# Kernel optimization log

Hardware: AMD Instinct MI355X
Metric: run time of the kernel (lower is better)

## Reference

```python
import jax, jax.numpy as jnp
import numpy as np

N_NODES = 100000
N_EDGES = 3200000
IN_CH, HID, OUT_CH = 512, 16, 64


def gcn_conv(x, src, dst, W, b, n_nodes):
    """GCNConv: x @ W, then sym-normalized aggregation with self-loops."""
    xw = x @ W  # [N, F_out]
    loop = jnp.arange(n_nodes, dtype=src.dtype)
    s = jnp.concatenate([src, loop])  # sources (messages gathered here)
    d = jnp.concatenate([dst, loop])  # targets (messages scattered here)
    deg = jax.ops.segment_sum(jnp.ones_like(d, dtype=xw.dtype), d, num_segments=n_nodes)
    dinv = jnp.where(deg > 0, jax.lax.rsqrt(deg), 0.0)
    norm = dinv[s] * dinv[d]  # [E+N]
    msgs = xw[s] * norm[:, None]  # gather + scale
    out = jax.ops.segment_sum(msgs, d, num_segments=n_nodes)
    return out + b


def setup_inputs() -> dict:
    key = jax.random.key(0)
    k1, k2, k3, k4, k5 = jax.random.split(key, 5)
    x = jax.random.normal(k1, (N_NODES, IN_CH), dtype=jnp.float32)
    edge_index = jax.random.randint(k2, (2, N_EDGES), 0, N_NODES, dtype=jnp.int32)
    # Glorot-style init for GCNConv linear weights, zero bias (PyG default)
    W1 = jax.random.normal(k3, (IN_CH, HID), dtype=jnp.float32) * (1.0 / np.sqrt(IN_CH))
    b1 = jnp.zeros((HID,), dtype=jnp.float32)
    W2 = jax.random.normal(k4, (HID, OUT_CH), dtype=jnp.float32) * (1.0 / np.sqrt(HID))
    b2 = jnp.zeros((OUT_CH,), dtype=jnp.float32)
    return {"x": x, "edge_index": edge_index, "W1": W1, "b1": b1, "W2": W2, "b2": b2}


def reference(x, edge_index, W1, b1, W2, b2):
    # eval mode: dropout(p=0.5) is identity
    src, dst = edge_index[0], edge_index[1]
    h = gcn_conv(x, src, dst, W1, b1, N_NODES)
    h = jax.nn.relu(h)
    out = gcn_conv(h, src, dst, W2, b2, N_NODES)
    return out
```

## Files before the change

### kernel.cpp

```cpp
#include <hip/hip_runtime.h>

#define N_NODES 100000
#define N_EDGES 3200000
#define IN_CH 512
#define HID 16
#define OUT_CH 64

#define NB1 98
#define CAP1 34816
#define LEAF 64
#define CAP2 2560
#define NLEAF 1563
#define NLEAF_SLOTS (NB1 * 16)
#define BIN1_CHUNK 4096
#define BIN1_BLOCKS ((N_EDGES + BIN1_CHUNK - 1) / BIN1_CHUNK)
#define BIN2_SPLIT 9
#define BIN2_CHUNK 3872

__device__ __forceinline__ float4 f4add(float4 a, float4 b) {
    return float4{a.x + b.x, a.y + b.y, a.z + b.z, a.w + b.w};
}
__device__ __forceinline__ float4 f4fma(float s, float4 w, float4 a) {
    return float4{a.x + s * w.x, a.y + s * w.y, a.z + s * w.z, a.w + s * w.w};
}


__global__ void k_init_bcur(int* bcur1, int* bcur2) {
    int i = blockIdx.x * blockDim.x + threadIdx.x;
    if (i < NB1) bcur1[i] = i * CAP1;
    if (i < NLEAF_SLOTS) bcur2[i] = i * CAP2;
}


__global__ __launch_bounds__(256) void k_bin1(const int* __restrict__ src,
                                              const int* __restrict__ dst,
                                              int* __restrict__ pairs1,
                                              int* __restrict__ bcur1) {
    __shared__ int cnt[NB1];
    __shared__ int base[NB1];
    const int tid = threadIdx.x;
    const int lo = blockIdx.x * BIN1_CHUNK;
    const int hi = min(lo + BIN1_CHUNK, N_EDGES);
    if (tid < NB1) cnt[tid] = 0;
    __syncthreads();
    for (int i = lo + tid; i < hi; i += 256) {
        int d = __builtin_nontemporal_load(dst + i);
        atomicAdd(&cnt[d >> 10], 1);
    }
    __syncthreads();
    if (tid < NB1 && cnt[tid] > 0) base[tid] = atomicAdd(&bcur1[tid], cnt[tid]);
    __syncthreads();
    if (tid < NB1) cnt[tid] = 0;
    __syncthreads();
    for (int i = lo + tid; i < hi; i += 256) {
        int d = __builtin_nontemporal_load(dst + i);
        int s = __builtin_nontemporal_load(src + i);
        int b = d >> 10;
        int r = atomicAdd(&cnt[b], 1);
        pairs1[base[b] + r] = (s << 10) | (d & 1023);
    }
}


__global__ __launch_bounds__(256) void k_bin2(const int* __restrict__ pairs1,
                                              const int* __restrict__ bcur1,
                                              int* __restrict__ pairs2,
                                              int* __restrict__ bcur2) {
    __shared__ int cnt[16];
    __shared__ int base[16];
    const int b = blockIdx.x / BIN2_SPLIT;
    const int s = blockIdx.x % BIN2_SPLIT;
    const int tid = threadIdx.x;
    const int len = bcur1[b] - b * CAP1;
    const int lo = b * CAP1 + min(s * BIN2_CHUNK, len);
    const int hi = b * CAP1 + min((s + 1) * BIN2_CHUNK, len);
    if (tid < 16) cnt[tid] = 0;
    __syncthreads();
    for (int i = lo + tid; i < hi; i += 256)
        atomicAdd(&cnt[(pairs1[i] & 1023) >> 6], 1);
    __syncthreads();
    if (tid < 16 && cnt[tid] > 0) base[tid] = atomicAdd(&bcur2[b * 16 + tid], cnt[tid]);
    __syncthreads();
    if (tid < 16) cnt[tid] = 0;
    __syncthreads();
    for (int i = lo + tid; i < hi; i += 256) {
        int e = pairs1[i];
        int l = (e & 1023) >> 6;
        int r = atomicAdd(&cnt[l], 1);
        pairs2[base[l] + r] = e;
    }
}


__global__ __launch_bounds__(256) void k_leafscan(const int* __restrict__ bcur2,
                                                  int* __restrict__ leafoff) {
    __shared__ int sm[256];
    __shared__ int carry;
    const int tid = threadIdx.x;
    if (tid == 0) carry = 0;
    __syncthreads();
    for (int r = 0; r < (NLEAF_SLOTS + 255) / 256; ++r) {
        int idx = r * 256 + tid;
        int v = (idx < NLEAF_SLOTS) ? (bcur2[idx] - idx * CAP2) : 0;
        sm[tid] = v;
        __syncthreads();
        for (int st = 1; st < 256; st <<= 1) {
            int t = (tid >= st) ? sm[tid - st] : 0;
            __syncthreads();
            sm[tid] += t;
            __syncthreads();
        }
        if (idx < NLEAF_SLOTS) leafoff[idx] = carry + sm[tid] - v;
        int tot = sm[255];
        __syncthreads();
        if (tid == 0) carry += tot;
        __syncthreads();
    }
}


__global__ __launch_bounds__(256) void k_scatter2(const int* __restrict__ pairs2,
                                                  const int* __restrict__ bcur2,
                                                  const int* __restrict__ leafoff,
                                                  int* __restrict__ off,
                                                  int* __restrict__ deg,
                                                  float* __restrict__ dinv,
                                                  int* __restrict__ csr) {
    __shared__ int cnt[LEAF];
    __shared__ int lcur[LEAF];
    __shared__ int buf[CAP2];
    const int leaf = blockIdx.x;
    const int tid = threadIdx.x;
    const int base2 = leaf * CAP2;
    const int len = min(bcur2[leaf] - base2, CAP2);
    const int obase = leafoff[leaf];
    if (tid < LEAF) cnt[tid] = 0;
    __syncthreads();
    for (int i = tid; i < len; i += 256)
        atomicAdd(&cnt[pairs2[base2 + i] & 63], 1);
    __syncthreads();
    if (tid < LEAF) {
        int v = cnt[tid];
        int s = v;
        for (int d = 1; d < LEAF; d <<= 1) {
            int t = __shfl_up(s, d, 64);
            if (tid >= d) s += t;
        }
        int excl = s - v;
        lcur[tid] = excl;
        int node = leaf * LEAF + tid;
        if (node < N_NODES) {
            off[node] = obase + excl;
            deg[node] = 1 + v;
            dinv[node] = rsqrtf((float)(1 + v));
        }
    }
    __syncthreads();
    for (int i = tid; i < len; i += 256) {
        int e = pairs2[base2 + i];
        int p = atomicAdd(&lcur[e & 63], 1);
        buf[p] = e >> 10;
    }
    __syncthreads();
    for (int i = tid; i < len; i += 256)
        csr[obase + i] = buf[i];
}


#define G1_BS 256
#define G1_NODES 128
#define G1_KT 64
#define G1_STRIDE (G1_KT + 4)

__global__ __launch_bounds__(G1_BS) void k_gemm1(const float* __restrict__ x,
                                                 const float* __restrict__ W1,
                                                 const float* __restrict__ dinv,
                                                 float* __restrict__ y1) {
    __shared__ float xt[G1_NODES * G1_STRIDE];
    __shared__ float wt[G1_KT * HID];
    const int tid = threadIdx.x;
    const int nl = tid >> 2;
    const int cg = tid & 3;
    const int node_base = blockIdx.x * G1_NODES;

    float4 acc0 = {0.f, 0.f, 0.f, 0.f};
    float4 acc1 = {0.f, 0.f, 0.f, 0.f};

    for (int kt = 0; kt < IN_CH; kt += G1_KT) {
        __syncthreads();
        for (int j = 0; j < 8; ++j) {
            int f4 = j * G1_BS + tid;
            int r = f4 >> 4;
            int c4 = f4 & 15;
            int gr = node_base + r;
            float4 v = {0.f, 0.f, 0.f, 0.f};
            if (gr < N_NODES)
                v = *(const float4*)(x + (size_t)gr * IN_CH + kt + c4 * 4);
            *(float4*)(xt + r * G1_STRIDE + c4 * 4) = v;
        }
        {
            int r = tid >> 2;
            int c4 = tid & 3;
            *(float4*)(wt + r * HID + c4 * 4) =
                *(const float4*)(W1 + (size_t)(kt + r) * HID + c4 * 4);
        }
        __syncthreads();

        for (int kk = 0; kk < G1_KT; kk += 4) {
            float4 x0 = *(const float4*)(xt + nl * G1_STRIDE + kk);
            float4 x1 = *(const float4*)(xt + (nl + 64) * G1_STRIDE + kk);
            float4 w0 = *(const float4*)(wt + (kk + 0) * HID + cg * 4);
            float4 w1 = *(const float4*)(wt + (kk + 1) * HID + cg * 4);
            float4 w2 = *(const float4*)(wt + (kk + 2) * HID + cg * 4);
            float4 w3 = *(const float4*)(wt + (kk + 3) * HID + cg * 4);
            acc0 = f4fma(x0.x, w0, acc0); acc0 = f4fma(x0.y, w1, acc0);
            acc0 = f4fma(x0.z, w2, acc0); acc0 = f4fma(x0.w, w3, acc0);
            acc1 = f4fma(x1.x, w0, acc1); acc1 = f4fma(x1.y, w1, acc1);
            acc1 = f4fma(x1.z, w2, acc1); acc1 = f4fma(x1.w, w3, acc1);
        }
    }

    int n0 = node_base + nl;
    int n1 = n0 + 64;
    if (n0 < N_NODES) {
        float dv = dinv[n0];
        float4 o = {acc0.x * dv, acc0.y * dv, acc0.z * dv, acc0.w * dv};
        *(float4*)(y1 + (size_t)n0 * HID + cg * 4) = o;
    }
    if (n1 < N_NODES) {
        float dv = dinv[n1];
        float4 o = {acc1.x * dv, acc1.y * dv, acc1.z * dv, acc1.w * dv};
        *(float4*)(y1 + (size_t)n1 * HID + cg * 4) = o;
    }
}


__global__ __launch_bounds__(256) void k_layer1(const float* __restrict__ y1,
                                                const int* __restrict__ off,
                                                const int* __restrict__ deg,
                                                const int* __restrict__ csr,
                                                const float* __restrict__ dinv,
                                                const float* __restrict__ b1,
                                                float* __restrict__ y2) {
    int t = blockIdx.x * blockDim.x + threadIdx.x;
    int n = t >> 2;
    int cg = t & 3;
    if (n >= N_NODES) return;
    int base = off[n];
    int cnt = deg[n] - 1;
    float4 a0 = {0,0,0,0}, a1 = {0,0,0,0}, a2 = {0,0,0,0}, a3 = {0,0,0,0};
    int p = 0;
    for (; p + 4 <= cnt; p += 4) {
        int s0 = csr[base + p + 0];
        int s1 = csr[base + p + 1];
        int s2 = csr[base + p + 2];
        int s3 = csr[base + p + 3];
        a0 = f4add(a0, *(const float4*)(y1 + (size_t)s0 * HID + cg * 4));
        a1 = f4add(a1, *(const float4*)(y1 + (size_t)s1 * HID + cg * 4));
        a2 = f4add(a2, *(const float4*)(y1 + (size_t)s2 * HID + cg * 4));
        a3 = f4add(a3, *(const float4*)(y1 + (size_t)s3 * HID + cg * 4));
    }
    for (; p < cnt; ++p)
        a0 = f4add(a0, *(const float4*)(y1 + (size_t)csr[base + p] * HID + cg * 4));
    float4 acc = f4add(f4add(a0, a1), f4add(a2, a3));
    float dv = dinv[n];
    float4 self = *(const float4*)(y1 + (size_t)n * HID + cg * 4);
    float4 b = ((const float4*)b1)[cg];
    float4 h;
    h.x = fmaxf(dv * (acc.x + self.x) + b.x, 0.f) * dv;
    h.y = fmaxf(dv * (acc.y + self.y) + b.y, 0.f) * dv;
    h.z = fmaxf(dv * (acc.z + self.z) + b.z, 0.f) * dv;
    h.w = fmaxf(dv * (acc.w + self.w) + b.w, 0.f) * dv;
    *(float4*)(y2 + (size_t)n * HID + cg * 4) = h;
}


__global__ __launch_bounds__(256) void k_layer2(const float* __restrict__ y2,
                                                const int* __restrict__ off,
                                                const int* __restrict__ deg,
                                                const int* __restrict__ csr,
                                                const float* __restrict__ dinv,
                                                const float* __restrict__ W2,
                                                const float* __restrict__ b2,
                                                float* __restrict__ out) {
    __shared__ float w2[HID * OUT_CH];
    __shared__ float bs[OUT_CH];
    int tid = threadIdx.x;
    for (int j = tid; j < HID * OUT_CH; j += 256) w2[j] = W2[j];
    if (tid < OUT_CH) bs[tid] = b2[tid];
    __syncthreads();

    int t = blockIdx.x * blockDim.x + tid;
    int n = t >> 2;
    int cg = t & 3;
    if (n >= N_NODES) return;
    int base = off[n];
    int cnt = deg[n] - 1;
    float4 a0 = {0,0,0,0}, a1 = {0,0,0,0}, a2 = {0,0,0,0}, a3 = {0,0,0,0};
    int p = 0;
    for (; p + 4 <= cnt; p += 4) {
        int s0 = csr[base + p + 0];
        int s1 = csr[base + p + 1];
        int s2 = csr[base + p + 2];
        int s3 = csr[base + p + 3];
        a0 = f4add(a0, *(const float4*)(y2 + (size_t)s0 * HID + cg * 4));
        a1 = f4add(a1, *(const float4*)(y2 + (size_t)s1 * HID + cg * 4));
        a2 = f4add(a2, *(const float4*)(y2 + (size_t)s2 * HID + cg * 4));
        a3 = f4add(a3, *(const float4*)(y2 + (size_t)s3 * HID + cg * 4));
    }
    for (; p < cnt; ++p)
        a0 = f4add(a0, *(const float4*)(y2 + (size_t)csr[base + p] * HID + cg * 4));
    float4 acc = f4add(f4add(a0, a1), f4add(a2, a3));
    float dv = dinv[n];
    float4 self = *(const float4*)(y2 + (size_t)n * HID + cg * 4);
    float4 z4 = {dv * (acc.x + self.x), dv * (acc.y + self.y),
                 dv * (acc.z + self.z), dv * (acc.w + self.w)};

    int lane = tid & 63;
    int lbase = lane & ~3;
    float z[16];
    for (int j = 0; j < 4; ++j) {
        z[j * 4 + 0] = __shfl(z4.x, lbase + j, 64);
        z[j * 4 + 1] = __shfl(z4.y, lbase + j, 64);
        z[j * 4 + 2] = __shfl(z4.z, lbase + j, 64);
        z[j * 4 + 3] = __shfl(z4.w, lbase + j, 64);
    }

    float4 o0 = ((const float4*)bs)[cg * 4 + 0];
    float4 o1 = ((const float4*)bs)[cg * 4 + 1];
    float4 o2 = ((const float4*)bs)[cg * 4 + 2];
    float4 o3 = ((const float4*)bs)[cg * 4 + 3];
    for (int cc = 0; cc < HID; ++cc) {
        const float* wr = w2 + cc * OUT_CH + cg * 16;
        float zz = z[cc];
        o0 = f4fma(zz, *(const float4*)(wr + 0), o0);
        o1 = f4fma(zz, *(const float4*)(wr + 4), o1);
        o2 = f4fma(zz, *(const float4*)(wr + 8), o2);
        o3 = f4fma(zz, *(const float4*)(wr + 12), o3);
    }
    float* orow = out + (size_t)n * OUT_CH + cg * 16;
    *(float4*)(orow + 0) = o0;
    *(float4*)(orow + 4) = o1;
    *(float4*)(orow + 8) = o2;
    *(float4*)(orow + 12) = o3;
}


extern "C" void kernel_launch(void* const* d_in, const int* in_sizes, int n_in,
                              void* d_out, int out_size, void* d_ws, size_t ws_size,
                              hipStream_t stream) {
    const float* x  = (const float*)d_in[0];
    const int*   ei = (const int*)d_in[1];
    const float* W1 = (const float*)d_in[2];
    const float* b1 = (const float*)d_in[3];
    const float* W2 = (const float*)d_in[4];
    const float* b2 = (const float*)d_in[5];
    float* out = (float*)d_out;

    const int* src = ei;
    const int* dst = ei + N_EDGES;

    char* w = (char*)d_ws;
    const size_t SN = 409600;
    int*   deg      = (int*)(w);
    float* dinv     = (float*)(w + SN);
    int*   off      = (int*)(w + 2 * SN);
    int*   bcur1    = (int*)(w + 3 * SN);
    int*   bcur2    = (int*)(w + 3 * SN + 8192);
    int*   leafoff  = (int*)(w + 3 * SN + 16384);
    char*  regB     = w + 4 * SN;
    int*   pairs1   = (int*)regB;
    int*   csr      = (int*)regB;
    char*  regC     = regB + (size_t)NB1 * CAP1 * 4;
    int*   pairs2   = (int*)regC;
    float* y1       = (float*)regC;
    float* y2       = (float*)(regC + 6553600);

    k_init_bcur<<<(NLEAF_SLOTS + 255) / 256, 256, 0, stream>>>(bcur1, bcur2);
    k_bin1<<<BIN1_BLOCKS, 256, 0, stream>>>(src, dst, pairs1, bcur1);
    k_bin2<<<NB1 * BIN2_SPLIT, 256, 0, stream>>>(pairs1, bcur1, pairs2, bcur2);
    k_leafscan<<<1, 256, 0, stream>>>(bcur2, leafoff);
    k_scatter2<<<NLEAF, 256, 0, stream>>>(pairs2, bcur2, leafoff, off, deg, dinv, csr);
    k_gemm1<<<(N_NODES + G1_NODES - 1) / G1_NODES, G1_BS, 0, stream>>>(x, W1, dinv, y1);
    k_layer1<<<(N_NODES * 4 + 255) / 256, 256, 0, stream>>>(y1, off, deg, csr, dinv, b1, y2);
    k_layer2<<<(N_NODES * 4 + 255) / 256, 256, 0, stream>>>(y2, off, deg, csr, dinv, W2, b2, out);
}
```

Measured before the change: 248.5 us.

## Split hidden features into two half-width arrays for cache-resident gather aggregation

Stores the 16-wide layer-1 projection as two separate 8-float arrays (3.2 MB each), so each aggregation pass gathers from a smaller table that can stay resident in cache. Each layer's aggregation is run as two passes, one per half, and the layer-2 W2 projection moves into a separate GEMM kernel that reads an intermediate z buffer. The deg array is dropped in favour of off[n+1]-off[n] plus an inline rsqrt. The cost is re-reading the CSR index array twice per layer, extra kernel launches, and an extra write and read of z.

```diff
diff --git a/kernel.cpp b/kernel.cpp
--- a/kernel.cpp
+++ b/kernel.cpp
@@ -25,10 +25,11 @@
 }
 
 
-__global__ void k_init_bcur(int* bcur1, int* bcur2) {
+__global__ void k_init_bcur(int* bcur1, int* bcur2, int* off) {
     int i = blockIdx.x * blockDim.x + threadIdx.x;
     if (i < NB1) bcur1[i] = i * CAP1;
     if (i < NLEAF_SLOTS) bcur2[i] = i * CAP2;
+    if (i == 0) off[N_NODES] = N_EDGES;
 }
 
 
@@ -123,7 +124,6 @@
                                                   const int* __restrict__ bcur2,
                                                   const int* __restrict__ leafoff,
                                                   int* __restrict__ off,
-                                                  int* __restrict__ deg,
                                                   float* __restrict__ dinv,
                                                   int* __restrict__ csr) {
     __shared__ int cnt[LEAF];
@@ -151,7 +151,6 @@
         int node = leaf * LEAF + tid;
         if (node < N_NODES) {
             off[node] = obase + excl;
-            deg[node] = 1 + v;
             dinv[node] = rsqrtf((float)(1 + v));
         }
     }
@@ -175,13 +174,16 @@
 __global__ __launch_bounds__(G1_BS) void k_gemm1(const float* __restrict__ x,
                                                  const float* __restrict__ W1,
                                                  const float* __restrict__ dinv,
-                                                 float* __restrict__ y1) {
+                                                 float* __restrict__ y1a,
+                                                 float* __restrict__ y1b) {
     __shared__ float xt[G1_NODES * G1_STRIDE];
     __shared__ float wt[G1_KT * HID];
     const int tid = threadIdx.x;
     const int nl = tid >> 2;
     const int cg = tid & 3;
     const int node_base = blockIdx.x * G1_NODES;
+    float* yh = (cg & 2) ? y1b : y1a;
+    const int hc = (cg & 1) * 4;
 
     float4 acc0 = {0.f, 0.f, 0.f, 0.f};
     float4 acc1 = {0.f, 0.f, 0.f, 0.f};
@@ -225,29 +227,28 @@
     if (n0 < N_NODES) {
         float dv = dinv[n0];
         float4 o = {acc0.x * dv, acc0.y * dv, acc0.z * dv, acc0.w * dv};
-        *(float4*)(y1 + (size_t)n0 * HID + cg * 4) = o;
+        *(float4*)(yh + (size_t)n0 * 8 + hc) = o;
     }
     if (n1 < N_NODES) {
         float dv = dinv[n1];
         float4 o = {acc1.x * dv, acc1.y * dv, acc1.z * dv, acc1.w * dv};
-        *(float4*)(y1 + (size_t)n1 * HID + cg * 4) = o;
-    }
-}
-
-
-__global__ __launch_bounds__(256) void k_layer1(const float* __restrict__ y1,
-                                                const int* __restrict__ off,
-                                                const int* __restrict__ deg,
-                                                const int* __restrict__ csr,
-                                                const float* __restrict__ dinv,
-                                                const float* __restrict__ b1,
-                                                float* __restrict__ y2) {
+        *(float4*)(yh + (size_t)n1 * 8 + hc) = o;
+    }
+}
+
+
+__global__ __launch_bounds__(256) void k_agg1(const float* __restrict__ yh,
+                                              const int* __restrict__ off,
+                                              const int* __restrict__ csr,
+                                              const float* __restrict__ b1,
+                                              const int half,
+                                              float* __restrict__ y2h) {
     int t = blockIdx.x * blockDim.x + threadIdx.x;
-    int n = t >> 2;
-    int cg = t & 3;
+    int n = t >> 1;
     if (n >= N_NODES) return;
+    int hc = (t & 1) * 4;
     int base = off[n];
-    int cnt = deg[n] - 1;
+    int cnt = off[n + 1] - base;
     float4 a0 = {0,0,0,0}, a1 = {0,0,0,0}, a2 = {0,0,0,0}, a3 = {0,0,0,0};
     int p = 0;
     for (; p + 4 <= cnt; p += 4) {
@@ -255,47 +256,37 @@
         int s1 = csr[base + p + 1];
         int s2 = csr[base + p + 2];
         int s3 = csr[base + p + 3];
-        a0 = f4add(a0, *(const float4*)(y1 + (size_t)s0 * HID + cg * 4));
-        a1 = f4add(a1, *(const float4*)(y1 + (size_t)s1 * HID + cg * 4));
-        a2 = f4add(a2, *(const float4*)(y1 + (size_t)s2 * HID + cg * 4));
-        a3 = f4add(a3, *(const float4*)(y1 + (size_t)s3 * HID + cg * 4));
+        a0 = f4add(a0, *(const float4*)(yh + (size_t)s0 * 8 + hc));
+        a1 = f4add(a1, *(const float4*)(yh + (size_t)s1 * 8 + hc));
+        a2 = f4add(a2, *(const float4*)(yh + (size_t)s2 * 8 + hc));
+        a3 = f4add(a3, *(const float4*)(yh + (size_t)s3 * 8 + hc));
     }
     for (; p < cnt; ++p)
-        a0 = f4add(a0, *(const float4*)(y1 + (size_t)csr[base + p] * HID + cg * 4));
+        a0 = f4add(a0, *(const float4*)(yh + (size_t)csr[base + p] * 8 + hc));
     float4 acc = f4add(f4add(a0, a1), f4add(a2, a3));
-    float dv = dinv[n];
-    float4 self = *(const float4*)(y1 + (size_t)n * HID + cg * 4);
-    float4 b = ((const float4*)b1)[cg];
+    float dv = rsqrtf((float)(cnt + 1));
+    float4 self = *(const float4*)(yh + (size_t)n * 8 + hc);
+    float4 b = *(const float4*)(b1 + half * 8 + hc);
     float4 h;
     h.x = fmaxf(dv * (acc.x + self.x) + b.x, 0.f) * dv;
     h.y = fmaxf(dv * (acc.y + self.y) + b.y, 0.f) * dv;
     h.z = fmaxf(dv * (acc.z + self.z) + b.z, 0.f) * dv;
     h.w = fmaxf(dv * (acc.w + self.w) + b.w, 0.f) * dv;
-    *(float4*)(y2 + (size_t)n * HID + cg * 4) = h;
-}
-
-
-__global__ __launch_bounds__(256) void k_layer2(const float* __restrict__ y2,
-                                                const int* __restrict__ off,
-                                                const int* __restrict__ deg,
-                                                const int* __restrict__ csr,
-                                                const float* __restrict__ dinv,
-                                                const float* __restrict__ W2,
-                                                const float* __restrict__ b2,
-                                                float* __restrict__ out) {
-    __shared__ float w2[HID * OUT_CH];
-    __shared__ float bs[OUT_CH];
-    int tid = threadIdx.x;
-    for (int j = tid; j < HID * OUT_CH; j += 256) w2[j] = W2[j];
-    if (tid < OUT_CH) bs[tid] = b2[tid];
-    __syncthreads();
-
-    int t = blockIdx.x * blockDim.x + tid;
-    int n = t >> 2;
-    int cg = t & 3;
+    *(float4*)(y2h + (size_t)n * 8 + hc) = h;
+}
+
+
+__global__ __launch_bounds__(256) void k_agg2(const float* __restrict__ yh,
+                                              const int* __restrict__ off,
+                                              const int* __restrict__ csr,
+                                              const int half,
+                                              float* __restrict__ z) {
+    int t = blockIdx.x * blockDim.x + threadIdx.x;
+    int n = t >> 1;
     if (n >= N_NODES) return;
+    int hc = (t & 1) * 4;
     int base = off[n];
-    int cnt = deg[n] - 1;
+    int cnt = off[n + 1] - base;
     float4 a0 = {0,0,0,0}, a1 = {0,0,0,0}, a2 = {0,0,0,0}, a3 = {0,0,0,0};
     int p = 0;
     for (; p + 4 <= cnt; p += 4) {
@@ -303,42 +294,57 @@
         int s1 = csr[base + p + 1];
         int s2 = csr[base + p + 2];
         int s3 = csr[base + p + 3];
-        a0 = f4add(a0, *(const float4*)(y2 + (size_t)s0 * HID + cg * 4));
-        a1 = f4add(a1, *(const float4*)(y2 + (size_t)s1 * HID + cg * 4));
-        a2 = f4add(a2, *(const float4*)(y2 + (size_t)s2 * HID + cg * 4));
-        a3 = f4add(a3, *(const float4*)(y2 + (size_t)s3 * HID + cg * 4));
+        a0 = f4add(a0, *(const float4*)(yh + (size_t)s0 * 8 + hc));
+        a1 = f4add(a1, *(const float4*)(yh + (size_t)s1 * 8 + hc));
+        a2 = f4add(a2, *(const float4*)(yh + (size_t)s2 * 8 + hc));
+        a3 = f4add(a3, *(const float4*)(yh + (size_t)s3 * 8 + hc));
     }
     for (; p < cnt; ++p)
-        a0 = f4add(a0, *(const float4*)(y2 + (size_t)csr[base + p] * HID + cg * 4));
+        a0 = f4add(a0, *(const float4*)(yh + (size_t)csr[base + p] * 8 + hc));
     float4 acc = f4add(f4add(a0, a1), f4add(a2, a3));
-    float dv = dinv[n];
-    float4 self = *(const float4*)(y2 + (size_t)n * HID + cg * 4);
-    float4 z4 = {dv * (acc.x + self.x), dv * (acc.y + self.y),
+    float dv = rsqrtf((float)(cnt + 1));
+    float4 self = *(const float4*)(yh + (size_t)n * 8 + hc);
+    float4 zv = {dv * (acc.x + self.x), dv * (acc.y + self.y),
                  dv * (acc.z + self.z), dv * (acc.w + self.w)};
-
-    int lane = tid & 63;
-    int lbase = lane & ~3;
-    float z[16];
-    for (int j = 0; j < 4; ++j) {
-        z[j * 4 + 0] = __shfl(z4.x, lbase + j, 64);
-        z[j * 4 + 1] = __shfl(z4.y, lbase + j, 64);
-        z[j * 4 + 2] = __shfl(z4.z, lbase + j, 64);
-        z[j * 4 + 3] = __shfl(z4.w, lbase + j, 64);
-    }
-
-    float4 o0 = ((const float4*)bs)[cg * 4 + 0];
-    float4 o1 = ((const float4*)bs)[cg * 4 + 1];
-    float4 o2 = ((const float4*)bs)[cg * 4 + 2];
-    float4 o3 = ((const float4*)bs)[cg * 4 + 3];
+    *(float4*)(z + (size_t)n * HID + half * 8 + hc) = zv;
+}
+
+
+__global__ __launch_bounds__(256) void k_gemm2(const float* __restrict__ z,
+                                               const float* __restrict__ W2,
+                                               const float* __restrict__ b2,
+                                               float* __restrict__ out) {
+    __shared__ float w2[HID * OUT_CH];
+    __shared__ float bs[OUT_CH];
+    int tid = threadIdx.x;
+    for (int j = tid; j < HID * OUT_CH; j += 256) w2[j] = W2[j];
+    if (tid < OUT_CH) bs[tid] = b2[tid];
+    __syncthreads();
+
+    int t = blockIdx.x * blockDim.x + tid;
+    int n = t >> 2;
+    int q = t & 3;
+    if (n >= N_NODES) return;
+    const float* zr = z + (size_t)n * HID;
+    float4 z0 = *(const float4*)(zr + 0);
+    float4 z1 = *(const float4*)(zr + 4);
+    float4 z2 = *(const float4*)(zr + 8);
+    float4 z3 = *(const float4*)(zr + 12);
+    float zz[16] = {z0.x, z0.y, z0.z, z0.w, z1.x, z1.y, z1.z, z1.w,
+                    z2.x, z2.y, z2.z, z2.w, z3.x, z3.y, z3.z, z3.w};
+    float4 o0 = ((const float4*)bs)[q * 4 + 0];
+    float4 o1 = ((const float4*)bs)[q * 4 + 1];
+    float4 o2 = ((const float4*)bs)[q * 4 + 2];
+    float4 o3 = ((const float4*)bs)[q * 4 + 3];
     for (int cc = 0; cc < HID; ++cc) {
-        const float* wr = w2 + cc * OUT_CH + cg * 16;
-        float zz = z[cc];
-        o0 = f4fma(zz, *(const float4*)(wr + 0), o0);
-        o1 = f4fma(zz, *(const float4*)(wr + 4), o1);
-        o2 = f4fma(zz, *(const float4*)(wr + 8), o2);
-        o3 = f4fma(zz, *(const float4*)(wr + 12), o3);
-    }
-    float* orow = out + (size_t)n * OUT_CH + cg * 16;
+        const float* wr = w2 + cc * OUT_CH + q * 16;
+        float s = zz[cc];
+        o0 = f4fma(s, *(const float4*)(wr + 0), o0);
+        o1 = f4fma(s, *(const float4*)(wr + 4), o1);
+        o2 = f4fma(s, *(const float4*)(wr + 8), o2);
+        o3 = f4fma(s, *(const float4*)(wr + 12), o3);
+    }
+    float* orow = out + (size_t)n * OUT_CH + q * 16;
     *(float4*)(orow + 0) = o0;
     *(float4*)(orow + 4) = o1;
     *(float4*)(orow + 8) = o2;
@@ -362,26 +368,34 @@
 
     char* w = (char*)d_ws;
     const size_t SN = 409600;
-    int*   deg      = (int*)(w);
-    float* dinv     = (float*)(w + SN);
-    int*   off      = (int*)(w + 2 * SN);
-    int*   bcur1    = (int*)(w + 3 * SN);
-    int*   bcur2    = (int*)(w + 3 * SN + 8192);
-    int*   leafoff  = (int*)(w + 3 * SN + 16384);
-    char*  regB     = w + 4 * SN;
+    float* dinv     = (float*)(w);
+    int*   off      = (int*)(w + SN);
+    int*   bcur1    = (int*)(w + 2 * SN);
+    int*   bcur2    = (int*)(w + 2 * SN + 8192);
+    int*   leafoff  = (int*)(w + 2 * SN + 16384);
+    char*  regB     = w + 3 * SN;
     int*   pairs1   = (int*)regB;
     int*   csr      = (int*)regB;
     char*  regC     = regB + (size_t)NB1 * CAP1 * 4;
     int*   pairs2   = (int*)regC;
-    float* y1       = (float*)regC;
-    float* y2       = (float*)(regC + 6553600);
-
-    k_init_bcur<<<(NLEAF_SLOTS + 255) / 256, 256, 0, stream>>>(bcur1, bcur2);
+    float* y1a      = (float*)regC;
+    float* y1b      = (float*)(regC + 3200000);
+    float* z        = (float*)(regC + 6400000);
+    char*  regD     = regC + (size_t)NLEAF_SLOTS * CAP2 * 4;
+    float* y2a      = (float*)regD;
+    float* y2b      = (float*)(regD + 3200000);
+
+    const int aggGrid = (N_NODES * 2 + 255) / 256;
+
+    k_init_bcur<<<(NLEAF_SLOTS + 255) / 256, 256, 0, stream>>>(bcur1, bcur2, off);
     k_bin1<<<BIN1_BLOCKS, 256, 0, stream>>>(src, dst, pairs1, bcur1);
     k_bin2<<<NB1 * BIN2_SPLIT, 256, 0, stream>>>(pairs1, bcur1, pairs2, bcur2);
     k_leafscan<<<1, 256, 0, stream>>>(bcur2, leafoff);
-    k_scatter2<<<NLEAF, 256, 0, stream>>>(pairs2, bcur2, leafoff, off, deg, dinv, csr);
-    k_gemm1<<<(N_NODES + G1_NODES - 1) / G1_NODES, G1_BS, 0, stream>>>(x, W1, dinv, y1);
-    k_layer1<<<(N_NODES * 4 + 255) / 256, 256, 0, stream>>>(y1, off, deg, csr, dinv, b1, y2);
-    k_layer2<<<(N_NODES * 4 + 255) / 256, 256, 0, stream>>>(y2, off, deg, csr, dinv, W2, b2, out);
-}
+    k_scatter2<<<NLEAF, 256, 0, stream>>>(pairs2, bcur2, leafoff, off, dinv, csr);
+    k_gemm1<<<(N_NODES + G1_NODES - 1) / G1_NODES, G1_BS, 0, stream>>>(x, W1, dinv, y1a, y1b);
+    k_agg1<<<aggGrid, 256, 0, stream>>>(y1a, off, csr, b1, 0, y2a);
+    k_agg1<<<aggGrid, 256, 0, stream>>>(y1b, off, csr, b1, 1, y2b);
+    k_agg2<<<aggGrid, 256, 0, stream>>>(y2a, off, csr, 0, z);
+    k_agg2<<<aggGrid, 256, 0, stream>>>(y2b, off, csr, 1, z);
+    k_gemm2<<<(N_NODES * 4 + 255) / 256, 256, 0, stream>>>(z, W2, b2, out);
+}
```

After: 287.8 us. +15.8%, slower.

## Store hidden features as bf16 and derive degree from CSR offsets

Applied to the files above, without the earlier changes.

Intermediate node features y1 and y2 are packed to bf16 with round-to-nearest-even, which halves the bytes moved by the random gathers in both aggregation layers. The separate degree and dinv arrays are dropped from the layer kernels: the count comes from off[n+1]-off[n] and rsqrt is recomputed in place, with a sentinel written at off[N_NODES]. Nontemporal stores are used for the outputs. Accuracy drops to bf16 precision for the intermediate features.

```diff
diff --git a/kernel.cpp b/kernel.cpp
--- a/kernel.cpp
+++ b/kernel.cpp
@@ -17,18 +17,34 @@
 #define BIN2_SPLIT 9
 #define BIN2_CHUNK 3872
 
-__device__ __forceinline__ float4 f4add(float4 a, float4 b) {
-    return float4{a.x + b.x, a.y + b.y, a.z + b.z, a.w + b.w};
-}
-__device__ __forceinline__ float4 f4fma(float s, float4 w, float4 a) {
-    return float4{a.x + s * w.x, a.y + s * w.y, a.z + s * w.z, a.w + s * w.w};
-}
-
-
-__global__ void k_init_bcur(int* bcur1, int* bcur2) {
+typedef float f4 __attribute__((ext_vector_type(4)));
+typedef unsigned int v2u __attribute__((ext_vector_type(2)));
+
+__device__ __forceinline__ unsigned rne(float f) {
+    unsigned u = __float_as_uint(f);
+    return (u + 0x7fffu + ((u >> 16) & 1u)) >> 16;
+}
+__device__ __forceinline__ v2u pk4(f4 f) {
+    v2u r;
+    r.x = rne(f.x) | (rne(f.y) << 16);
+    r.y = rne(f.z) | (rne(f.w) << 16);
+    return r;
+}
+__device__ __forceinline__ f4 up4(v2u v) {
+    f4 r;
+    r.x = __uint_as_float(v.x << 16);
+    r.y = __uint_as_float(v.x & 0xffff0000u);
+    r.z = __uint_as_float(v.y << 16);
+    r.w = __uint_as_float(v.y & 0xffff0000u);
+    return r;
+}
+
+
+__global__ void k_init_bcur(int* bcur1, int* bcur2, int* off) {
     int i = blockIdx.x * blockDim.x + threadIdx.x;
     if (i < NB1) bcur1[i] = i * CAP1;
     if (i < NLEAF_SLOTS) bcur2[i] = i * CAP2;
+    if (i == 0) off[N_NODES] = N_EDGES;
 }
 
 
@@ -123,7 +139,6 @@
                                                   const int* __restrict__ bcur2,
                                                   const int* __restrict__ leafoff,
                                                   int* __restrict__ off,
-                                                  int* __restrict__ deg,
                                                   float* __restrict__ dinv,
                                                   int* __restrict__ csr) {
     __shared__ int cnt[LEAF];
@@ -151,7 +166,6 @@
         int node = leaf * LEAF + tid;
         if (node < N_NODES) {
             off[node] = obase + excl;
-            deg[node] = 1 + v;
             dinv[node] = rsqrtf((float)(1 + v));
         }
     }
@@ -175,7 +189,7 @@
 __global__ __launch_bounds__(G1_BS) void k_gemm1(const float* __restrict__ x,
                                                  const float* __restrict__ W1,
                                                  const float* __restrict__ dinv,
-                                                 float* __restrict__ y1) {
+                                                 unsigned short* __restrict__ y1) {
     __shared__ float xt[G1_NODES * G1_STRIDE];
     __shared__ float wt[G1_KT * HID];
     const int tid = threadIdx.x;
@@ -183,40 +197,40 @@
     const int cg = tid & 3;
     const int node_base = blockIdx.x * G1_NODES;
 
-    float4 acc0 = {0.f, 0.f, 0.f, 0.f};
-    float4 acc1 = {0.f, 0.f, 0.f, 0.f};
+    f4 acc0 = {0.f, 0.f, 0.f, 0.f};
+    f4 acc1 = {0.f, 0.f, 0.f, 0.f};
 
     for (int kt = 0; kt < IN_CH; kt += G1_KT) {
         __syncthreads();
         for (int j = 0; j < 8; ++j) {
-            int f4 = j * G1_BS + tid;
-            int r = f4 >> 4;
-            int c4 = f4 & 15;
+            int f = j * G1_BS + tid;
+            int r = f >> 4;
+            int c4 = f & 15;
             int gr = node_base + r;
-            float4 v = {0.f, 0.f, 0.f, 0.f};
+            f4 v = {0.f, 0.f, 0.f, 0.f};
             if (gr < N_NODES)
-                v = *(const float4*)(x + (size_t)gr * IN_CH + kt + c4 * 4);
-            *(float4*)(xt + r * G1_STRIDE + c4 * 4) = v;
+                v = *(const f4*)(x + (size_t)gr * IN_CH + kt + c4 * 4);
+            *(f4*)(xt + r * G1_STRIDE + c4 * 4) = v;
         }
         {
             int r = tid >> 2;
             int c4 = tid & 3;
-            *(float4*)(wt + r * HID + c4 * 4) =
-                *(const float4*)(W1 + (size_t)(kt + r) * HID + c4 * 4);
+            *(f4*)(wt + r * HID + c4 * 4) =
+                *(const f4*)(W1 + (size_t)(kt + r) * HID + c4 * 4);
         }
         __syncthreads();
 
         for (int kk = 0; kk < G1_KT; kk += 4) {
-            float4 x0 = *(const float4*)(xt + nl * G1_STRIDE + kk);
-            float4 x1 = *(const float4*)(xt + (nl + 64) * G1_STRIDE + kk);
-            float4 w0 = *(const float4*)(wt + (kk + 0) * HID + cg * 4);
-            float4 w1 = *(const float4*)(wt + (kk + 1) * HID + cg * 4);
-            float4 w2 = *(const float4*)(wt + (kk + 2) * HID + cg * 4);
-            float4 w3 = *(const float4*)(wt + (kk + 3) * HID + cg * 4);
-            acc0 = f4fma(x0.x, w0, acc0); acc0 = f4fma(x0.y, w1, acc0);
-            acc0 = f4fma(x0.z, w2, acc0); acc0 = f4fma(x0.w, w3, acc0);
-            acc1 = f4fma(x1.x, w0, acc1); acc1 = f4fma(x1.y, w1, acc1);
-            acc1 = f4fma(x1.z, w2, acc1); acc1 = f4fma(x1.w, w3, acc1);
+            f4 x0 = *(const f4*)(xt + nl * G1_STRIDE + kk);
+            f4 x1 = *(const f4*)(xt + (nl + 64) * G1_STRIDE + kk);
+            f4 w0 = *(const f4*)(wt + (kk + 0) * HID + cg * 4);
+            f4 w1 = *(const f4*)(wt + (kk + 1) * HID + cg * 4);
+            f4 w2 = *(const f4*)(wt + (kk + 2) * HID + cg * 4);
+            f4 w3 = *(const f4*)(wt + (kk + 3) * HID + cg * 4);
+            acc0 += x0.x * w0; acc0 += x0.y * w1;
+            acc0 += x0.z * w2; acc0 += x0.w * w3;
+            acc1 += x1.x * w0; acc1 += x1.y * w1;
+            acc1 += x1.z * w2; acc1 += x1.w * w3;
         }
     }
 
@@ -224,62 +238,58 @@
     int n1 = n0 + 64;
     if (n0 < N_NODES) {
         float dv = dinv[n0];
-        float4 o = {acc0.x * dv, acc0.y * dv, acc0.z * dv, acc0.w * dv};
-        *(float4*)(y1 + (size_t)n0 * HID + cg * 4) = o;
+        __builtin_nontemporal_store(pk4(acc0 * dv),
+            (v2u*)(y1 + (size_t)n0 * HID + cg * 4));
     }
     if (n1 < N_NODES) {
         float dv = dinv[n1];
-        float4 o = {acc1.x * dv, acc1.y * dv, acc1.z * dv, acc1.w * dv};
-        *(float4*)(y1 + (size_t)n1 * HID + cg * 4) = o;
-    }
-}
-
-
-__global__ __launch_bounds__(256) void k_layer1(const float* __restrict__ y1,
+        __builtin_nontemporal_store(pk4(acc1 * dv),
+            (v2u*)(y1 + (size_t)n1 * HID + cg * 4));
+    }
+}
+
+
+__global__ __launch_bounds__(256) void k_layer1(const unsigned short* __restrict__ y1,
                                                 const int* __restrict__ off,
-                                                const int* __restrict__ deg,
                                                 const int* __restrict__ csr,
-                                                const float* __restrict__ dinv,
                                                 const float* __restrict__ b1,
-                                                float* __restrict__ y2) {
+                                                unsigned short* __restrict__ y2) {
     int t = blockIdx.x * blockDim.x + threadIdx.x;
     int n = t >> 2;
     int cg = t & 3;
     if (n >= N_NODES) return;
     int base = off[n];
-    int cnt = deg[n] - 1;
-    float4 a0 = {0,0,0,0}, a1 = {0,0,0,0}, a2 = {0,0,0,0}, a3 = {0,0,0,0};
+    int cnt = off[n + 1] - base;
+    f4 a0 = {0,0,0,0}, a1 = {0,0,0,0}, a2 = {0,0,0,0}, a3 = {0,0,0,0};
     int p = 0;
     for (; p + 4 <= cnt; p += 4) {
         int s0 = csr[base + p + 0];
         int s1 = csr[base + p + 1];
         int s2 = csr[base + p + 2];
         int s3 = csr[base + p + 3];
-        a0 = f4add(a0, *(const float4*)(y1 + (size_t)s0 * HID + cg * 4));
-        a1 = f4add(a1, *(const float4*)(y1 + (size_t)s1 * HID + cg * 4));
-        a2 = f4add(a2, *(const float4*)(y1 + (size_t)s2 * HID + cg * 4));
-        a3 = f4add(a3, *(const float4*)(y1 + (size_t)s3 * HID + cg * 4));
+        a0 += up4(*(const v2u*)(y1 + (size_t)s0 * HID + cg * 4));
+        a1 += up4(*(const v2u*)(y1 + (size_t)s1 * HID + cg * 4));
+        a2 += up4(*(const v2u*)(y1 + (size_t)s2 * HID + cg * 4));
+        a3 += up4(*(const v2u*)(y1 + (size_t)s3 * HID + cg * 4));
     }
     for (; p < cnt; ++p)
-        a0 = f4add(a0, *(const float4*)(y1 + (size_t)csr[base + p] * HID + cg * 4));
-    float4 acc = f4add(f4add(a0, a1), f4add(a2, a3));
-    float dv = dinv[n];
-    float4 self = *(const float4*)(y1 + (size_t)n * HID + cg * 4);
-    float4 b = ((const float4*)b1)[cg];
-    float4 h;
+        a0 += up4(*(const v2u*)(y1 + (size_t)csr[base + p] * HID + cg * 4));
+    f4 acc = (a0 + a1) + (a2 + a3);
+    float dv = rsqrtf((float)(cnt + 1));
+    f4 self = up4(*(const v2u*)(y1 + (size_t)n * HID + cg * 4));
+    f4 b = ((const f4*)b1)[cg];
+    f4 h;
     h.x = fmaxf(dv * (acc.x + self.x) + b.x, 0.f) * dv;
     h.y = fmaxf(dv * (acc.y + self.y) + b.y, 0.f) * dv;
     h.z = fmaxf(dv * (acc.z + self.z) + b.z, 0.f) * dv;
     h.w = fmaxf(dv * (acc.w + self.w) + b.w, 0.f) * dv;
-    *(float4*)(y2 + (size_t)n * HID + cg * 4) = h;
-}
-
-
-__global__ __launch_bounds__(256) void k_layer2(const float* __restrict__ y2,
+    __builtin_nontemporal_store(pk4(h), (v2u*)(y2 + (size_t)n * HID + cg * 4));
+}
+
+
+__global__ __launch_bounds__(256) void k_layer2(const unsigned short* __restrict__ y2,
                                                 const int* __restrict__ off,
-                                                const int* __restrict__ deg,
                                                 const int* __restrict__ csr,
-                                                const float* __restrict__ dinv,
                                                 const float* __restrict__ W2,
                                                 const float* __restrict__ b2,
                                                 float* __restrict__ out) {
@@ -295,26 +305,26 @@
     int cg = t & 3;
     if (n >= N_NODES) return;
     int base = off[n];
-    int cnt = deg[n] - 1;
-    float4 a0 = {0,0,0,0}, a1 = {0,0,0,0}, a2 = {0,0,0,0}, a3 = {0,0,0,0};
+    int cnt = off[n + 1] - base;
+    f4 a0 = {0,0,0,0}, a1 = {0,0,0,0}, a2 = {0,0,0,0}, a3 = {0,0,0,0};
     int p = 0;
     for (; p + 4 <= cnt; p += 4) {
         int s0 = csr[base + p + 0];
         int s1 = csr[base + p + 1];
         int s2 = csr[base + p + 2];
         int s3 = csr[base + p + 3];
-        a0 = f4add(a0, *(const float4*)(y2 + (size_t)s0 * HID + cg * 4));
-        a1 = f4add(a1, *(const float4*)(y2 + (size_t)s1 * HID + cg * 4));
-        a2 = f4add(a2, *(const float4*)(y2 + (size_t)s2 * HID + cg * 4));
-        a3 = f4add(a3, *(const float4*)(y2 + (size_t)s3 * HID + cg * 4));
+        a0 += up4(*(const v2u*)(y2 + (size_t)s0 * HID + cg * 4));
+        a1 += up4(*(const v2u*)(y2 + (size_t)s1 * HID + cg * 4));
+        a2 += up4(*(const v2u*)(y2 + (size_t)s2 * HID + cg * 4));
+        a3 += up4(*(const v2u*)(y2 + (size_t)s3 * HID + cg * 4));
     }
     for (; p < cnt; ++p)
-        a0 = f4add(a0, *(const float4*)(y2 + (size_t)csr[base + p] * HID + cg * 4));
-    float4 acc = f4add(f4add(a0, a1), f4add(a2, a3));
-    float dv = dinv[n];
-    float4 self = *(const float4*)(y2 + (size_t)n * HID + cg * 4);
-    float4 z4 = {dv * (acc.x + self.x), dv * (acc.y + self.y),
-                 dv * (acc.z + self.z), dv * (acc.w + self.w)};
+        a0 += up4(*(const v2u*)(y2 + (size_t)csr[base + p] * HID + cg * 4));
+    f4 acc = (a0 + a1) + (a2 + a3);
+    float dv = rsqrtf((float)(cnt + 1));
+    f4 self = up4(*(const v2u*)(y2 + (size_t)n * HID + cg * 4));
+    f4 z4 = {dv * (acc.x + self.x), dv * (acc.y + self.y),
+             dv * (acc.z + self.z), dv * (acc.w + self.w)};
 
     int lane = tid & 63;
     int lbase = lane & ~3;
@@ -326,23 +336,23 @@
         z[j * 4 + 3] = __shfl(z4.w, lbase + j, 64);
     }
 
-    float4 o0 = ((const float4*)bs)[cg * 4 + 0];
-    float4 o1 = ((const float4*)bs)[cg * 4 + 1];
-    float4 o2 = ((const float4*)bs)[cg * 4 + 2];
-    float4 o3 = ((const float4*)bs)[cg * 4 + 3];
+    f4 o0 = ((const f4*)bs)[cg * 4 + 0];
+    f4 o1 = ((const f4*)bs)[cg * 4 + 1];
+    f4 o2 = ((const f4*)bs)[cg * 4 + 2];
+    f4 o3 = ((const f4*)bs)[cg * 4 + 3];
     for (int cc = 0; cc < HID; ++cc) {
         const float* wr = w2 + cc * OUT_CH + cg * 16;
         float zz = z[cc];
-        o0 = f4fma(zz, *(const float4*)(wr + 0), o0);
-        o1 = f4fma(zz, *(const float4*)(wr + 4), o1);
-        o2 = f4fma(zz, *(const float4*)(wr + 8), o2);
-        o3 = f4fma(zz, *(const float4*)(wr + 12), o3);
+        o0 += zz * *(const f4*)(wr + 0);
+        o1 += zz * *(const f4*)(wr + 4);
+        o2 += zz * *(const f4*)(wr + 8);
+        o3 += zz * *(const f4*)(wr + 12);
     }
     float* orow = out + (size_t)n * OUT_CH + cg * 16;
-    *(float4*)(orow + 0) = o0;
-    *(float4*)(orow + 4) = o1;
-    *(float4*)(orow + 8) = o2;
-    *(float4*)(orow + 12) = o3;
+    __builtin_nontemporal_store(o0, (f4*)(orow + 0));
+    __builtin_nontemporal_store(o1, (f4*)(orow + 4));
+    __builtin_nontemporal_store(o2, (f4*)(orow + 8));
+    __builtin_nontemporal_store(o3, (f4*)(orow + 12));
 }
 
 
@@ -362,26 +372,25 @@
 
     char* w = (char*)d_ws;
     const size_t SN = 409600;
-    int*   deg      = (int*)(w);
-    float* dinv     = (float*)(w + SN);
-    int*   off      = (int*)(w + 2 * SN);
-    int*   bcur1    = (int*)(w + 3 * SN);
-    int*   bcur2    = (int*)(w + 3 * SN + 8192);
-    int*   leafoff  = (int*)(w + 3 * SN + 16384);
-    char*  regB     = w + 4 * SN;
+    float* dinv     = (float*)(w);
+    int*   off      = (int*)(w + SN);
+    int*   bcur1    = (int*)(w + 2 * SN);
+    int*   bcur2    = (int*)(w + 2 * SN + 8192);
+    int*   leafoff  = (int*)(w + 2 * SN + 16384);
+    char*  regB     = w + 3 * SN;
     int*   pairs1   = (int*)regB;
     int*   csr      = (int*)regB;
     char*  regC     = regB + (size_t)NB1 * CAP1 * 4;
     int*   pairs2   = (int*)regC;
-    float* y1       = (float*)regC;
-    float* y2       = (float*)(regC + 6553600);
-
-    k_init_bcur<<<(NLEAF_SLOTS + 255) / 256, 256, 0, stream>>>(bcur1, bcur2);
+    unsigned short* y1 = (unsigned short*)regC;
+    unsigned short* y2 = (unsigned short*)(regC + 3200000);
+
+    k_init_bcur<<<(NLEAF_SLOTS + 255) / 256, 256, 0, stream>>>(bcur1, bcur2, off);
     k_bin1<<<BIN1_BLOCKS, 256, 0, stream>>>(src, dst, pairs1, bcur1);
     k_bin2<<<NB1 * BIN2_SPLIT, 256, 0, stream>>>(pairs1, bcur1, pairs2, bcur2);
     k_leafscan<<<1, 256, 0, stream>>>(bcur2, leafoff);
-    k_scatter2<<<NLEAF, 256, 0, stream>>>(pairs2, bcur2, leafoff, off, deg, dinv, csr);
+    k_scatter2<<<NLEAF, 256, 0, stream>>>(pairs2, bcur2, leafoff, off, dinv, csr);
     k_gemm1<<<(N_NODES + G1_NODES - 1) / G1_NODES, G1_BS, 0, stream>>>(x, W1, dinv, y1);
-    k_layer1<<<(N_NODES * 4 + 255) / 256, 256, 0, stream>>>(y1, off, deg, csr, dinv, b1, y2);
-    k_layer2<<<(N_NODES * 4 + 255) / 256, 256, 0, stream>>>(y2, off, deg, csr, dinv, W2, b2, out);
-}
+    k_layer1<<<(N_NODES * 4 + 255) / 256, 256, 0, stream>>>(y1, off, csr, b1, y2);
+    k_layer2<<<(N_NODES * 4 + 255) / 256, 256, 0, stream>>>(y2, off, csr, W2, b2, out);
+}
```

Result: faster. 208.9 us (-15.9%).
